# Kernel tuning notes

Hardware: AMD Instinct MI355X
Metric: run time of the kernel (lower is better)

## Reference

```python
import jax, jax.numpy as jnp
import numpy as np


def hard_sigmoid(x):
    # Keras hard_sigmoid: clip(0.2*x + 0.5, 0, 1)
    return jnp.clip(0.2 * x + 0.5, 0.0, 1.0)


def setup_inputs() -> dict:
    key = jax.random.key(0)
    k1, k2, k3 = jax.random.split(key, 3)
    B, H, W, C = 32, 64, 64, 256
    x = jax.random.normal(k1, (B, H, W, C), dtype=jnp.float32)
    # glorot_uniform over (C, W, H): fan_in = W (last-two matmul dims are W x H)
    limit = np.sqrt(6.0 / (W + H)).astype(np.float32)
    Wq = jax.random.uniform(k2, (C, W, H), minval=-limit, maxval=limit, dtype=jnp.float32)
    Wk = jax.random.uniform(k3, (C, W, H), minval=-limit, maxval=limit, dtype=jnp.float32)
    return {"x": x, "Wq": Wq, "Wk": Wk}


def reference(x, Wq, Wk):
    # x: [B, H, W, C] -> [B, C, H, W]
    xt = jnp.transpose(x, (0, 3, 1, 2))
    # projections: [B,C,H,W] @ [C,W,H] (broadcast over B) -> [B,C,H,H]
    q = hard_sigmoid(jnp.einsum('bchw,cwk->bchk', xt, Wq))
    K = jnp.tanh(jnp.einsum('bchw,cwk->bchk', xt, Wk))
    # scores: q @ K^T over last two dims -> [B,C,H,H]
    qk = hard_sigmoid(jnp.einsum('bchk,bcmk->bchm', q, K))
    qk = jax.nn.softmax(qk, axis=-1)
    # output: [B,C,H,W] @ [B,C,W(==H),H] -> [B,C,H,H]
    out = jnp.einsum('bchw,bcwm->bchm', xt, qk)
    # back to channels-last [B,H,W,C]
    return jnp.transpose(out, (0, 2, 3, 1))
```

## Files before the change

### kernel.cpp

```cpp
#include <hip/hip_runtime.h>


typedef short short8 __attribute__((ext_vector_type(8)));
typedef float floatx4 __attribute__((ext_vector_type(4)));
typedef unsigned int uint;

__device__ __forceinline__ uint cvtpk(float a, float b) {
  uint r;
  asm("v_cvt_pk_bf16_f32 %0, %1, %2" : "=v"(r) : "v"(a), "v"(b));
  return r;
}
__device__ __forceinline__ short8 u4s8(uint a, uint b, uint c, uint d) {
  union { uint u[4]; short8 s; } t;
  t.u[0] = a; t.u[1] = b; t.u[2] = c; t.u[3] = d;
  return t.s;
}
__device__ __forceinline__ float hsg(float x) {
  return fminf(fmaxf(0.2f * x + 0.5f, 0.f), 1.f);
}

__device__ __forceinline__ void pl32swap(uint A, uint C, uint& lo, uint& hi, int quad) {
#if __has_builtin(__builtin_amdgcn_permlane32_swap)
  auto r = __builtin_amdgcn_permlane32_swap(A, C, false, false);
  lo = (uint)r[0]; hi = (uint)r[1];
#else
  uint sA = __shfl_xor(A, 32), sC = __shfl_xor(C, 32);
  bool up = quad >= 2;
  lo = up ? sC : A;
  hi = up ? C : sA;
#endif
}
__device__ __forceinline__ void pl16swap(uint A, uint C, uint& lo, uint& hi, int quad) {
#if __has_builtin(__builtin_amdgcn_permlane16_swap)
  auto r = __builtin_amdgcn_permlane16_swap(A, C, false, false);
  lo = (uint)r[0]; hi = (uint)r[1];
#else
  uint sA = (uint)__builtin_amdgcn_ds_swizzle((int)A, 0x401F);
  uint sC = (uint)__builtin_amdgcn_ds_swizzle((int)C, 0x401F);
  bool odd = quad & 1;
  lo = odd ? sC : A;
  hi = odd ? C : sA;
#endif
}
__device__ __forceinline__ short8 xchg4(uint A, uint B, uint C, uint D, int quad) {
  uint Ap, Cp, Bp, Dp, t0, t1, t2, t3;
  pl32swap(A, C, Ap, Cp, quad);
  pl32swap(B, D, Bp, Dp, quad);
  pl16swap(Ap, Cp, t0, t2, quad);
  pl16swap(Bp, Dp, t1, t3, quad);
  return u4s8(t0, t1, t2, t3);
}

__global__ __launch_bounds__(256) void prep_w(const float* __restrict__ Wq,
                                              const float* __restrict__ Wk,
                                              unsigned short* __restrict__ ws) {
  __shared__ __align__(16) unsigned char sm[4 * 8704];
  const int tid = threadIdx.x, lane = tid & 63, wid = tid >> 6;
  const int task = blockIdx.x * 4 + wid;
  const int c = task & 255;
  const float* wp = ((task >> 8) ? Wk : Wq) + (size_t)c * 4096;
  unsigned char* buf = sm + wid * 8704;
  const int l15 = lane & 15, quad = lane >> 4;
#pragma unroll 4
  for (int j = 0; j < 16; ++j) {
    int f4 = j * 64 + lane;
    float4 v = *(const float4*)(wp + (size_t)f4 * 4);
    int w = f4 >> 4, k0 = (f4 & 15) << 2;
    uint2 pk; pk.x = cvtpk(v.x, v.y); pk.y = cvtpk(v.z, v.w);
    *(uint2*)(buf + w * 136 + k0 * 2) = pk;
  }
  unsigned short* dst = ws + (size_t)task * 4096;
#pragma unroll
  for (int kt = 0; kt < 4; ++kt)
#pragma unroll
    for (int ks = 0; ks < 2; ++ks) {
      const unsigned short* p = (const unsigned short*)buf + (ks * 32 + quad * 8) * 68 + (kt * 16 + l15);
      short8 af = u4s8((uint)p[0]   | ((uint)p[68]  << 16),
                       (uint)p[136] | ((uint)p[204] << 16),
                       (uint)p[272] | ((uint)p[340] << 16),
                       (uint)p[408] | ((uint)p[476] << 16));
      *(short8*)(dst + ((kt * 2 + ks) * 64 + lane) * 8) = af;
    }
}

__global__ __launch_bounds__(512, 4) void fused_attn(
    const float* __restrict__ x, const unsigned short* __restrict__ wsp,
    float* __restrict__ out) {
  __shared__ __align__(16) unsigned char smem[8 * 8192];

  const int tid  = threadIdx.x;
  const int lane = tid & 63;
  const int wid  = tid >> 6;
  const int l15  = lane & 15;
  const int quad = lane >> 4;

  const int b   = blockIdx.x & 31;
  const int cg8 = blockIdx.x >> 5;
  const int c0  = cg8 << 3;
  const int c   = c0 + wid;

  unsigned char* buf0 = smem + wid * 8192;

  const short8* wqf = (const short8*)wsp + (size_t)c * 512;
  const short8* wkf = wqf + 256 * 512;

  short8 aq[4][2];
#pragma unroll
  for (int kt = 0; kt < 4; ++kt)
#pragma unroll
    for (int ks = 0; ks < 2; ++ks) aq[kt][ks] = wqf[(kt * 2 + ks) * 64 + lane];

  {
    const int ch4 = tid & 1, grp = tid >> 1;
    const float* xb = x + (size_t)b * 4096 * 256 + c0 + ch4 * 4;
#pragma unroll
    for (int bat = 0; bat < 2; ++bat) {
      float4 va[4], vb[4];
#pragma unroll
      for (int i = 0; i < 4; ++i) {
        int pair = (bat * 4 + i) * 256 + grp;
        int h = pair >> 5, w0 = (pair & 31) << 1;
        const float* src = xb + (size_t)(h * 64 + w0) * 256;
        va[i] = *(const float4*)src;
        vb[i] = *(const float4*)(src + 256);
      }
#pragma unroll
      for (int i = 0; i < 4; ++i) {
        int pair = (bat * 4 + i) * 256 + grp;
        int h = pair >> 5, w0 = (pair & 31) << 1;
        uint off = (uint)(h * 128 + (((w0 >> 3) ^ (h & 7)) << 4) + ((w0 & 7) << 1));
        unsigned char* base = smem + (size_t)(ch4 * 4) * 8192 + off;
        *(uint*)(base + 0 * 8192) = cvtpk(va[i].x, vb[i].x);
        *(uint*)(base + 1 * 8192) = cvtpk(va[i].y, vb[i].y);
        *(uint*)(base + 2 * 8192) = cvtpk(va[i].z, vb[i].z);
        *(uint*)(base + 3 * 8192) = cvtpk(va[i].w, vb[i].w);
      }
    }
  }
  __syncthreads();

  const floatx4 zero4 = {0.f, 0.f, 0.f, 0.f};
  floatx4 acc[16];

#pragma unroll
  for (int i = 0; i < 16; ++i) acc[i] = zero4;
#pragma unroll
  for (int ht = 0; ht < 4; ++ht) {
    int r = ht * 16 + l15;
    short8 x0 = *(const short8*)(buf0 + r * 128 + (((quad) ^ (r & 7)) << 4));
    short8 x1 = *(const short8*)(buf0 + r * 128 + (((4 + quad) ^ (r & 7)) << 4));
    __builtin_amdgcn_s_setprio(1);
#pragma unroll
    for (int kt = 0; kt < 4; ++kt) {
      acc[kt * 4 + ht] = __builtin_amdgcn_mfma_f32_16x16x32_bf16(aq[kt][0], x0, acc[kt * 4 + ht], 0, 0, 0);
      acc[kt * 4 + ht] = __builtin_amdgcn_mfma_f32_16x16x32_bf16(aq[kt][1], x1, acc[kt * 4 + ht], 0, 0, 0);
    }
    __builtin_amdgcn_s_setprio(0);
  }

  short8 qf[4][2];
#pragma unroll
  for (int ht = 0; ht < 4; ++ht) {
    uint s[4][2];
#pragma unroll
    for (int kt = 0; kt < 4; ++kt) {
      floatx4 a = acc[kt * 4 + ht];
      s[kt][0] = cvtpk(hsg(a[0]), hsg(a[1]));
      s[kt][1] = cvtpk(hsg(a[2]), hsg(a[3]));
    }
#pragma unroll
    for (int ks = 0; ks < 2; ++ks)
      qf[ht][ks] = xchg4(s[2 * ks][0], s[2 * ks][1], s[2 * ks + 1][0], s[2 * ks + 1][1], quad);
  }

#pragma unroll
  for (int i = 0; i < 16; ++i) acc[i] = zero4;
#pragma unroll
  for (int kt = 0; kt < 4; ++kt) {
    short8 a0 = wkf[(kt * 2 + 0) * 64 + lane];
    short8 a1 = wkf[(kt * 2 + 1) * 64 + lane];
    __builtin_amdgcn_s_setprio(1);
#pragma unroll
    for (int ht = 0; ht < 4; ++ht) {
      int r = ht * 16 + l15;
      short8 x0 = *(const short8*)(buf0 + r * 128 + (((quad) ^ (r & 7)) << 4));
      short8 x1 = *(const short8*)(buf0 + r * 128 + (((4 + quad) ^ (r & 7)) << 4));
      acc[kt * 4 + ht] = __builtin_amdgcn_mfma_f32_16x16x32_bf16(a0, x0, acc[kt * 4 + ht], 0, 0, 0);
      acc[kt * 4 + ht] = __builtin_amdgcn_mfma_f32_16x16x32_bf16(a1, x1, acc[kt * 4 + ht], 0, 0, 0);
    }
    __builtin_amdgcn_s_setprio(0);
  }
  short8 kf[4][2];
#pragma unroll
  for (int ht = 0; ht < 4; ++ht) {
    uint t[4][2];
#pragma unroll
    for (int kt = 0; kt < 4; ++kt) {
      floatx4 a = acc[kt * 4 + ht];
      float kv[4];
#pragma unroll
      for (int i = 0; i < 4; ++i) {
        float e = __expf(2.f * a[i]);
        kv[i] = 1.f - 2.f / (e + 1.f);
      }
      t[kt][0] = cvtpk(kv[0], kv[1]);
      t[kt][1] = cvtpk(kv[2], kv[3]);
    }
#pragma unroll
    for (int ks = 0; ks < 2; ++ks)
      kf[ht][ks] = xchg4(t[2 * ks][0], t[2 * ks][1], t[2 * ks + 1][0], t[2 * ks + 1][1], quad);
  }

  short8 sf[4][2];
#pragma unroll
  for (int ks2 = 0; ks2 < 2; ++ks2) {
    floatx4 a2[8];
#pragma unroll
    for (int i = 0; i < 8; ++i) a2[i] = zero4;
    __builtin_amdgcn_s_setprio(1);
#pragma unroll
    for (int mt = 0; mt < 4; ++mt)
#pragma unroll
      for (int wtl = 0; wtl < 2; ++wtl) {
        int wt = ks2 * 2 + wtl;
        a2[wtl * 4 + mt] = __builtin_amdgcn_mfma_f32_16x16x32_bf16(qf[wt][0], kf[mt][0], a2[wtl * 4 + mt], 0, 0, 0);
        a2[wtl * 4 + mt] = __builtin_amdgcn_mfma_f32_16x16x32_bf16(qf[wt][1], kf[mt][1], a2[wtl * 4 + mt], 0, 0, 0);
      }
    __builtin_amdgcn_s_setprio(0);
#pragma unroll
    for (int i = 0; i < 8; ++i)
#pragma unroll
      for (int j = 0; j < 4; ++j) a2[i][j] = __expf(hsg(a2[i][j]));
    float inv2[2][4];
#pragma unroll
    for (int wtl = 0; wtl < 2; ++wtl)
#pragma unroll
      for (int i = 0; i < 4; ++i) {
        float pp = a2[wtl * 4 + 0][i] + a2[wtl * 4 + 1][i] + a2[wtl * 4 + 2][i] + a2[wtl * 4 + 3][i];
        pp += __shfl_xor(pp, 1, 16);
        pp += __shfl_xor(pp, 2, 16);
        pp += __shfl_xor(pp, 4, 16);
        pp += __shfl_xor(pp, 8, 16);
        inv2[wtl][i] = 1.f / pp;
      }
#pragma unroll
    for (int mt = 0; mt < 4; ++mt) {
      uint s0 = cvtpk(a2[mt][0] * inv2[0][0], a2[mt][1] * inv2[0][1]);
      uint s1 = cvtpk(a2[mt][2] * inv2[0][2], a2[mt][3] * inv2[0][3]);
      uint s2 = cvtpk(a2[4 + mt][0] * inv2[1][0], a2[4 + mt][1] * inv2[1][1]);
      uint s3 = cvtpk(a2[4 + mt][2] * inv2[1][2], a2[4 + mt][3] * inv2[1][3]);
      sf[mt][ks2] = xchg4(s0, s1, s2, s3, quad);
    }
  }

#pragma unroll
  for (int i = 0; i < 16; ++i) acc[i] = zero4;
#pragma unroll
  for (int ht = 0; ht < 4; ++ht) {
    int r = ht * 16 + l15;
    short8 x0 = *(const short8*)(buf0 + r * 128 + (((quad) ^ (r & 7)) << 4));
    short8 x1 = *(const short8*)(buf0 + r * 128 + (((4 + quad) ^ (r & 7)) << 4));
    __builtin_amdgcn_s_setprio(1);
#pragma unroll
    for (int mt = 0; mt < 4; ++mt) {
      acc[mt * 4 + ht] = __builtin_amdgcn_mfma_f32_16x16x32_bf16(sf[mt][0], x0, acc[mt * 4 + ht], 0, 0, 0);
      acc[mt * 4 + ht] = __builtin_amdgcn_mfma_f32_16x16x32_bf16(sf[mt][1], x1, acc[mt * 4 + ht], 0, 0, 0);
    }
    __builtin_amdgcn_s_setprio(0);
  }
#pragma unroll
  for (int mt = 0; mt < 4; ++mt)
#pragma unroll
    for (int ht = 0; ht < 4; ++ht) {
      floatx4 a = acc[mt * 4 + ht];
      uint2 pk; pk.x = cvtpk(a[0], a[1]); pk.y = cvtpk(a[2], a[3]);
      int h = ht * 16 + l15;
      *(uint2*)(buf0 + h * 128 + ((((mt * 2 + (quad >> 1)) ^ (h & 7))) << 4) + ((quad & 1) << 3)) = pk;
    }
  __syncthreads();

  {
    const int ch4 = tid & 1, grp = tid >> 1;
    const size_t outbase = (size_t)b * 4096 * 256 + c0 + ch4 * 4;
#pragma unroll
    for (int rep = 0; rep < 4; ++rep) {
      int qidx = rep * 256 + grp;
      int h = qidx >> 4, mq = qidx & 15;
      uint loff = (uint)(h * 128 + ((((mq >> 1) ^ (h & 7))) << 4) + ((mq & 1) << 3));
      float vals[4][4];
#pragma unroll
      for (int j = 0; j < 4; ++j) {
        uint2 d = *(const uint2*)(smem + (size_t)(ch4 * 4 + j) * 8192 + loff);
        vals[j][0] = __uint_as_float(d.x << 16);
        vals[j][1] = __uint_as_float(d.x & 0xFFFF0000u);
        vals[j][2] = __uint_as_float(d.y << 16);
        vals[j][3] = __uint_as_float(d.y & 0xFFFF0000u);
      }
      float* op = out + outbase + (size_t)(h * 64 + mq * 4) * 256;
#pragma unroll
      for (int jj = 0; jj < 4; ++jj) {
        float4 v = {vals[0][jj], vals[1][jj], vals[2][jj], vals[3][jj]};
        *(float4*)(op + (size_t)jj * 256) = v;
      }
    }
  }
}

extern "C" void kernel_launch(void* const* d_in, const int* in_sizes, int n_in,
                              void* d_out, int out_size, void* d_ws, size_t ws_size,
                              hipStream_t stream) {
  const float* x  = (const float*)d_in[0];
  const float* Wq = (const float*)d_in[1];
  const float* Wk = (const float*)d_in[2];
  unsigned short* ws = (unsigned short*)d_ws;
  prep_w<<<dim3(128), dim3(256), 0, stream>>>(Wq, Wk, ws);
  fused_attn<<<dim3(1024), dim3(512), 0, stream>>>(x, ws, (float*)d_out);
}
```

Before: 300.4 us.

## Make fused attention persistent over four batches with prefetched x staging

Each block now handles four consecutive batch items for its 8-channel group instead of one, giving 256 blocks instead of 1024. The global loads of the next batch's x slice are issued during the current batch's MFMA phases, and a separate output buffer in doubled shared memory lets staging and writeback overlap. x fragments are held in registers and reused by all three matmuls instead of being reloaded from LDS. The cost is higher register and LDS pressure (launch bounds lowered to 2 blocks per CU, 128KB LDS) and fewer blocks available to hide latency.

```diff
diff --git a/kernel.cpp b/kernel.cpp
--- a/kernel.cpp
+++ b/kernel.cpp
@@ -4,6 +4,9 @@
 typedef short short8 __attribute__((ext_vector_type(8)));
 typedef float floatx4 __attribute__((ext_vector_type(4)));
 typedef unsigned int uint;
+
+#define BAR() do { asm volatile("s_waitcnt lgkmcnt(0)" ::: "memory"); \
+    __builtin_amdgcn_s_barrier(); __builtin_amdgcn_sched_barrier(0); } while (0)
 
 __device__ __forceinline__ uint cvtpk(float a, float b) {
   uint r;
@@ -49,6 +52,41 @@
   pl16swap(Ap, Cp, t0, t2, quad);
   pl16swap(Bp, Dp, t1, t3, quad);
   return u4s8(t0, t1, t2, t3);
+}
+
+__device__ __forceinline__ void stage_issue(const float* xb, int grp, int i0,
+                                            float4* va, float4* vb) {
+#pragma unroll
+  for (int i = 0; i < 4; ++i) {
+    int pair = (i0 + i) * 256 + grp;
+    int h = pair >> 5, w0 = (pair & 31) << 1;
+    const float* src = xb + (size_t)(h * 64 + w0) * 256;
+    va[i] = *(const float4*)src;
+    vb[i] = *(const float4*)(src + 256);
+  }
+}
+__device__ __forceinline__ void stage_commit(unsigned char* base0, int grp, int i0,
+                                             const float4* va, const float4* vb) {
+#pragma unroll
+  for (int i = 0; i < 4; ++i) {
+    int pair = (i0 + i) * 256 + grp;
+    int h = pair >> 5, w0 = (pair & 31) << 1;
+    uint off = (uint)(h * 128 + (((w0 >> 3) ^ (h & 7)) << 4) + ((w0 & 7) << 1));
+    *(uint*)(base0 + 0 * 8192 + off) = cvtpk(va[i].x, vb[i].x);
+    *(uint*)(base0 + 1 * 8192 + off) = cvtpk(va[i].y, vb[i].y);
+    *(uint*)(base0 + 2 * 8192 + off) = cvtpk(va[i].z, vb[i].z);
+    *(uint*)(base0 + 3 * 8192 + off) = cvtpk(va[i].w, vb[i].w);
+  }
+}
+__device__ __forceinline__ void ld_xf(const unsigned char* buf0, int l15, int quad,
+                                      short8 xf[4][2]) {
+#pragma unroll
+  for (int rt = 0; rt < 4; ++rt) {
+    int r = rt * 16 + l15;
+#pragma unroll
+    for (int ks = 0; ks < 2; ++ks)
+      xf[rt][ks] = *(const short8*)(buf0 + r * 128 + (((ks * 4 + quad) ^ (r & 7)) << 4));
+  }
 }
 
 __global__ __launch_bounds__(256) void prep_w(const float* __restrict__ Wq,
@@ -83,23 +121,27 @@
     }
 }
 
-__global__ __launch_bounds__(512, 4) void fused_attn(
+__global__ __launch_bounds__(512, 2) void fused_attn(
     const float* __restrict__ x, const unsigned short* __restrict__ wsp,
     float* __restrict__ out) {
-  __shared__ __align__(16) unsigned char smem[8 * 8192];
+  __shared__ __align__(16) unsigned char smem[2 * 8 * 8192];
 
   const int tid  = threadIdx.x;
   const int lane = tid & 63;
   const int wid  = tid >> 6;
   const int l15  = lane & 15;
   const int quad = lane >> 4;
-
-  const int b   = blockIdx.x & 31;
-  const int cg8 = blockIdx.x >> 5;
+  const int ch4  = tid & 1;
+  const int grp  = tid >> 1;
+
+  const int cg8 = blockIdx.x & 31;
+  const int bq  = blockIdx.x >> 5;
   const int c0  = cg8 << 3;
   const int c   = c0 + wid;
 
-  unsigned char* buf0 = smem + wid * 8192;
+  unsigned char* xbuf = smem + wid * 8192;
+  unsigned char* obuf = smem + 65536 + wid * 8192;
+  unsigned char* stb  = smem + ch4 * 32768;
 
   const short8* wqf = (const short8*)wsp + (size_t)c * 512;
   const short8* wkf = wqf + 256 * 512;
@@ -111,198 +153,192 @@
     for (int ks = 0; ks < 2; ++ks) aq[kt][ks] = wqf[(kt * 2 + ks) * 64 + lane];
 
   {
-    const int ch4 = tid & 1, grp = tid >> 1;
-    const float* xb = x + (size_t)b * 4096 * 256 + c0 + ch4 * 4;
-#pragma unroll
-    for (int bat = 0; bat < 2; ++bat) {
-      float4 va[4], vb[4];
-#pragma unroll
-      for (int i = 0; i < 4; ++i) {
-        int pair = (bat * 4 + i) * 256 + grp;
-        int h = pair >> 5, w0 = (pair & 31) << 1;
-        const float* src = xb + (size_t)(h * 64 + w0) * 256;
-        va[i] = *(const float4*)src;
-        vb[i] = *(const float4*)(src + 256);
-      }
-#pragma unroll
-      for (int i = 0; i < 4; ++i) {
-        int pair = (bat * 4 + i) * 256 + grp;
-        int h = pair >> 5, w0 = (pair & 31) << 1;
-        uint off = (uint)(h * 128 + (((w0 >> 3) ^ (h & 7)) << 4) + ((w0 & 7) << 1));
-        unsigned char* base = smem + (size_t)(ch4 * 4) * 8192 + off;
-        *(uint*)(base + 0 * 8192) = cvtpk(va[i].x, vb[i].x);
-        *(uint*)(base + 1 * 8192) = cvtpk(va[i].y, vb[i].y);
-        *(uint*)(base + 2 * 8192) = cvtpk(va[i].z, vb[i].z);
-        *(uint*)(base + 3 * 8192) = cvtpk(va[i].w, vb[i].w);
-      }
-    }
-  }
-  __syncthreads();
+    const float* xb = x + (size_t)(bq * 4) * 4096 * 256 + c0 + ch4 * 4;
+    float4 va[4], vb[4];
+    stage_issue(xb, grp, 0, va, vb);
+    stage_commit(stb, grp, 0, va, vb);
+    stage_issue(xb, grp, 4, va, vb);
+    stage_commit(stb, grp, 4, va, vb);
+  }
+  BAR();
+  short8 xf[4][2];
+  ld_xf(xbuf, l15, quad, xf);
+  BAR();
 
   const floatx4 zero4 = {0.f, 0.f, 0.f, 0.f};
-  floatx4 acc[16];
-
-#pragma unroll
-  for (int i = 0; i < 16; ++i) acc[i] = zero4;
-#pragma unroll
-  for (int ht = 0; ht < 4; ++ht) {
-    int r = ht * 16 + l15;
-    short8 x0 = *(const short8*)(buf0 + r * 128 + (((quad) ^ (r & 7)) << 4));
-    short8 x1 = *(const short8*)(buf0 + r * 128 + (((4 + quad) ^ (r & 7)) << 4));
+
+  for (int it = 0; it < 4; ++it) {
+    const bool pre = (it < 3);
+    const float* xbn = x + (size_t)(bq * 4 + it + 1) * 4096 * 256 + c0 + ch4 * 4;
+    float4 va[4], vb[4];
+    if (pre) stage_issue(xbn, grp, 0, va, vb);
+
+    short8 wkr[4][2];
+#pragma unroll
+    for (int kt = 0; kt < 4; ++kt)
+#pragma unroll
+      for (int ks = 0; ks < 2; ++ks) wkr[kt][ks] = wkf[(kt * 2 + ks) * 64 + lane];
+
+    floatx4 acc[16];
+
+#pragma unroll
+    for (int i = 0; i < 16; ++i) acc[i] = zero4;
     __builtin_amdgcn_s_setprio(1);
 #pragma unroll
-    for (int kt = 0; kt < 4; ++kt) {
-      acc[kt * 4 + ht] = __builtin_amdgcn_mfma_f32_16x16x32_bf16(aq[kt][0], x0, acc[kt * 4 + ht], 0, 0, 0);
-      acc[kt * 4 + ht] = __builtin_amdgcn_mfma_f32_16x16x32_bf16(aq[kt][1], x1, acc[kt * 4 + ht], 0, 0, 0);
-    }
+    for (int kt = 0; kt < 4; ++kt)
+#pragma unroll
+      for (int ht = 0; ht < 4; ++ht) {
+        acc[kt * 4 + ht] = __builtin_amdgcn_mfma_f32_16x16x32_bf16(aq[kt][0], xf[ht][0], acc[kt * 4 + ht], 0, 0, 0);
+        acc[kt * 4 + ht] = __builtin_amdgcn_mfma_f32_16x16x32_bf16(aq[kt][1], xf[ht][1], acc[kt * 4 + ht], 0, 0, 0);
+      }
     __builtin_amdgcn_s_setprio(0);
-  }
-
-  short8 qf[4][2];
-#pragma unroll
-  for (int ht = 0; ht < 4; ++ht) {
-    uint s[4][2];
-#pragma unroll
-    for (int kt = 0; kt < 4; ++kt) {
-      floatx4 a = acc[kt * 4 + ht];
-      s[kt][0] = cvtpk(hsg(a[0]), hsg(a[1]));
-      s[kt][1] = cvtpk(hsg(a[2]), hsg(a[3]));
-    }
-#pragma unroll
-    for (int ks = 0; ks < 2; ++ks)
-      qf[ht][ks] = xchg4(s[2 * ks][0], s[2 * ks][1], s[2 * ks + 1][0], s[2 * ks + 1][1], quad);
-  }
-
-#pragma unroll
-  for (int i = 0; i < 16; ++i) acc[i] = zero4;
-#pragma unroll
-  for (int kt = 0; kt < 4; ++kt) {
-    short8 a0 = wkf[(kt * 2 + 0) * 64 + lane];
-    short8 a1 = wkf[(kt * 2 + 1) * 64 + lane];
+
+    short8 qf[4][2];
+#pragma unroll
+    for (int ht = 0; ht < 4; ++ht) {
+      uint s[4][2];
+#pragma unroll
+      for (int kt = 0; kt < 4; ++kt) {
+        floatx4 a = acc[kt * 4 + ht];
+        s[kt][0] = cvtpk(hsg(a[0]), hsg(a[1]));
+        s[kt][1] = cvtpk(hsg(a[2]), hsg(a[3]));
+      }
+#pragma unroll
+      for (int ks = 0; ks < 2; ++ks)
+        qf[ht][ks] = xchg4(s[2 * ks][0], s[2 * ks][1], s[2 * ks + 1][0], s[2 * ks + 1][1], quad);
+    }
+
+    if (pre) {
+      stage_commit(stb, grp, 0, va, vb);
+      stage_issue(xbn, grp, 4, va, vb);
+    }
+
+#pragma unroll
+    for (int i = 0; i < 16; ++i) acc[i] = zero4;
     __builtin_amdgcn_s_setprio(1);
 #pragma unroll
+    for (int kt = 0; kt < 4; ++kt)
+#pragma unroll
+      for (int ht = 0; ht < 4; ++ht) {
+        acc[kt * 4 + ht] = __builtin_amdgcn_mfma_f32_16x16x32_bf16(wkr[kt][0], xf[ht][0], acc[kt * 4 + ht], 0, 0, 0);
+        acc[kt * 4 + ht] = __builtin_amdgcn_mfma_f32_16x16x32_bf16(wkr[kt][1], xf[ht][1], acc[kt * 4 + ht], 0, 0, 0);
+      }
+    __builtin_amdgcn_s_setprio(0);
+
+    short8 kf[4][2];
+#pragma unroll
     for (int ht = 0; ht < 4; ++ht) {
-      int r = ht * 16 + l15;
-      short8 x0 = *(const short8*)(buf0 + r * 128 + (((quad) ^ (r & 7)) << 4));
-      short8 x1 = *(const short8*)(buf0 + r * 128 + (((4 + quad) ^ (r & 7)) << 4));
-      acc[kt * 4 + ht] = __builtin_amdgcn_mfma_f32_16x16x32_bf16(a0, x0, acc[kt * 4 + ht], 0, 0, 0);
-      acc[kt * 4 + ht] = __builtin_amdgcn_mfma_f32_16x16x32_bf16(a1, x1, acc[kt * 4 + ht], 0, 0, 0);
-    }
+      uint t[4][2];
+#pragma unroll
+      for (int kt = 0; kt < 4; ++kt) {
+        floatx4 a = acc[kt * 4 + ht];
+        float kv[4];
+#pragma unroll
+        for (int i = 0; i < 4; ++i) {
+          float e = __expf(2.f * a[i]);
+          kv[i] = 1.f - 2.f / (e + 1.f);
+        }
+        t[kt][0] = cvtpk(kv[0], kv[1]);
+        t[kt][1] = cvtpk(kv[2], kv[3]);
+      }
+#pragma unroll
+      for (int ks = 0; ks < 2; ++ks)
+        kf[ht][ks] = xchg4(t[2 * ks][0], t[2 * ks][1], t[2 * ks + 1][0], t[2 * ks + 1][1], quad);
+    }
+
+    if (pre) stage_commit(stb, grp, 4, va, vb);
+
+    short8 sf[4][2];
+#pragma unroll
+    for (int ks2 = 0; ks2 < 2; ++ks2) {
+      floatx4 a2[8];
+#pragma unroll
+      for (int i = 0; i < 8; ++i) a2[i] = zero4;
+      __builtin_amdgcn_s_setprio(1);
+#pragma unroll
+      for (int mt = 0; mt < 4; ++mt)
+#pragma unroll
+        for (int wtl = 0; wtl < 2; ++wtl) {
+          int wt = ks2 * 2 + wtl;
+          a2[wtl * 4 + mt] = __builtin_amdgcn_mfma_f32_16x16x32_bf16(qf[wt][0], kf[mt][0], a2[wtl * 4 + mt], 0, 0, 0);
+          a2[wtl * 4 + mt] = __builtin_amdgcn_mfma_f32_16x16x32_bf16(qf[wt][1], kf[mt][1], a2[wtl * 4 + mt], 0, 0, 0);
+        }
+      __builtin_amdgcn_s_setprio(0);
+#pragma unroll
+      for (int i = 0; i < 8; ++i)
+#pragma unroll
+        for (int j = 0; j < 4; ++j) a2[i][j] = __expf(hsg(a2[i][j]));
+      float inv2[2][4];
+#pragma unroll
+      for (int wtl = 0; wtl < 2; ++wtl)
+#pragma unroll
+        for (int i = 0; i < 4; ++i) {
+          float pp = a2[wtl * 4 + 0][i] + a2[wtl * 4 + 1][i] + a2[wtl * 4 + 2][i] + a2[wtl * 4 + 3][i];
+          pp += __shfl_xor(pp, 1, 16);
+          pp += __shfl_xor(pp, 2, 16);
+          pp += __shfl_xor(pp, 4, 16);
+          pp += __shfl_xor(pp, 8, 16);
+          inv2[wtl][i] = 1.f / pp;
+        }
+#pragma unroll
+      for (int mt = 0; mt < 4; ++mt) {
+        uint s0 = cvtpk(a2[mt][0] * inv2[0][0], a2[mt][1] * inv2[0][1]);
+        uint s1 = cvtpk(a2[mt][2] * inv2[0][2], a2[mt][3] * inv2[0][3]);
+        uint s2 = cvtpk(a2[4 + mt][0] * inv2[1][0], a2[4 + mt][1] * inv2[1][1]);
+        uint s3 = cvtpk(a2[4 + mt][2] * inv2[1][2], a2[4 + mt][3] * inv2[1][3]);
+        sf[mt][ks2] = xchg4(s0, s1, s2, s3, quad);
+      }
+    }
+
+#pragma unroll
+    for (int i = 0; i < 16; ++i) acc[i] = zero4;
+    __builtin_amdgcn_s_setprio(1);
+#pragma unroll
+    for (int mt = 0; mt < 4; ++mt)
+#pragma unroll
+      for (int ht = 0; ht < 4; ++ht) {
+        acc[mt * 4 + ht] = __builtin_amdgcn_mfma_f32_16x16x32_bf16(sf[mt][0], xf[ht][0], acc[mt * 4 + ht], 0, 0, 0);
+        acc[mt * 4 + ht] = __builtin_amdgcn_mfma_f32_16x16x32_bf16(sf[mt][1], xf[ht][1], acc[mt * 4 + ht], 0, 0, 0);
+      }
     __builtin_amdgcn_s_setprio(0);
-  }
-  short8 kf[4][2];
-#pragma unroll
-  for (int ht = 0; ht < 4; ++ht) {
-    uint t[4][2];
-#pragma unroll
-    for (int kt = 0; kt < 4; ++kt) {
-      floatx4 a = acc[kt * 4 + ht];
-      float kv[4];
-#pragma unroll
-      for (int i = 0; i < 4; ++i) {
-        float e = __expf(2.f * a[i]);
-        kv[i] = 1.f - 2.f / (e + 1.f);
-      }
-      t[kt][0] = cvtpk(kv[0], kv[1]);
-      t[kt][1] = cvtpk(kv[2], kv[3]);
-    }
-#pragma unroll
-    for (int ks = 0; ks < 2; ++ks)
-      kf[ht][ks] = xchg4(t[2 * ks][0], t[2 * ks][1], t[2 * ks + 1][0], t[2 * ks + 1][1], quad);
-  }
-
-  short8 sf[4][2];
-#pragma unroll
-  for (int ks2 = 0; ks2 < 2; ++ks2) {
-    floatx4 a2[8];
-#pragma unroll
-    for (int i = 0; i < 8; ++i) a2[i] = zero4;
-    __builtin_amdgcn_s_setprio(1);
 #pragma unroll
     for (int mt = 0; mt < 4; ++mt)
 #pragma unroll
-      for (int wtl = 0; wtl < 2; ++wtl) {
-        int wt = ks2 * 2 + wtl;
-        a2[wtl * 4 + mt] = __builtin_amdgcn_mfma_f32_16x16x32_bf16(qf[wt][0], kf[mt][0], a2[wtl * 4 + mt], 0, 0, 0);
-        a2[wtl * 4 + mt] = __builtin_amdgcn_mfma_f32_16x16x32_bf16(qf[wt][1], kf[mt][1], a2[wtl * 4 + mt], 0, 0, 0);
-      }
-    __builtin_amdgcn_s_setprio(0);
-#pragma unroll
-    for (int i = 0; i < 8; ++i)
-#pragma unroll
-      for (int j = 0; j < 4; ++j) a2[i][j] = __expf(hsg(a2[i][j]));
-    float inv2[2][4];
-#pragma unroll
-    for (int wtl = 0; wtl < 2; ++wtl)
-#pragma unroll
-      for (int i = 0; i < 4; ++i) {
-        float pp = a2[wtl * 4 + 0][i] + a2[wtl * 4 + 1][i] + a2[wtl * 4 + 2][i] + a2[wtl * 4 + 3][i];
-        pp += __shfl_xor(pp, 1, 16);
-        pp += __shfl_xor(pp, 2, 16);
-        pp += __shfl_xor(pp, 4, 16);
-        pp += __shfl_xor(pp, 8, 16);
-        inv2[wtl][i] = 1.f / pp;
-      }
-#pragma unroll
-    for (int mt = 0; mt < 4; ++mt) {
-      uint s0 = cvtpk(a2[mt][0] * inv2[0][0], a2[mt][1] * inv2[0][1]);
-      uint s1 = cvtpk(a2[mt][2] * inv2[0][2], a2[mt][3] * inv2[0][3]);
-      uint s2 = cvtpk(a2[4 + mt][0] * inv2[1][0], a2[4 + mt][1] * inv2[1][1]);
-      uint s3 = cvtpk(a2[4 + mt][2] * inv2[1][2], a2[4 + mt][3] * inv2[1][3]);
-      sf[mt][ks2] = xchg4(s0, s1, s2, s3, quad);
-    }
-  }
-
-#pragma unroll
-  for (int i = 0; i < 16; ++i) acc[i] = zero4;
-#pragma unroll
-  for (int ht = 0; ht < 4; ++ht) {
-    int r = ht * 16 + l15;
-    short8 x0 = *(const short8*)(buf0 + r * 128 + (((quad) ^ (r & 7)) << 4));
-    short8 x1 = *(const short8*)(buf0 + r * 128 + (((4 + quad) ^ (r & 7)) << 4));
-    __builtin_amdgcn_s_setprio(1);
-#pragma unroll
-    for (int mt = 0; mt < 4; ++mt) {
-      acc[mt * 4 + ht] = __builtin_amdgcn_mfma_f32_16x16x32_bf16(sf[mt][0], x0, acc[mt * 4 + ht], 0, 0, 0);
-      acc[mt * 4 + ht] = __builtin_amdgcn_mfma_f32_16x16x32_bf16(sf[mt][1], x1, acc[mt * 4 + ht], 0, 0, 0);
-    }
-    __builtin_amdgcn_s_setprio(0);
-  }
-#pragma unroll
-  for (int mt = 0; mt < 4; ++mt)
-#pragma unroll
-    for (int ht = 0; ht < 4; ++ht) {
-      floatx4 a = acc[mt * 4 + ht];
-      uint2 pk; pk.x = cvtpk(a[0], a[1]); pk.y = cvtpk(a[2], a[3]);
-      int h = ht * 16 + l15;
-      *(uint2*)(buf0 + h * 128 + ((((mt * 2 + (quad >> 1)) ^ (h & 7))) << 4) + ((quad & 1) << 3)) = pk;
-    }
-  __syncthreads();
-
-  {
-    const int ch4 = tid & 1, grp = tid >> 1;
-    const size_t outbase = (size_t)b * 4096 * 256 + c0 + ch4 * 4;
-#pragma unroll
-    for (int rep = 0; rep < 4; ++rep) {
-      int qidx = rep * 256 + grp;
-      int h = qidx >> 4, mq = qidx & 15;
-      uint loff = (uint)(h * 128 + ((((mq >> 1) ^ (h & 7))) << 4) + ((mq & 1) << 3));
-      float vals[4][4];
-#pragma unroll
-      for (int j = 0; j < 4; ++j) {
-        uint2 d = *(const uint2*)(smem + (size_t)(ch4 * 4 + j) * 8192 + loff);
-        vals[j][0] = __uint_as_float(d.x << 16);
-        vals[j][1] = __uint_as_float(d.x & 0xFFFF0000u);
-        vals[j][2] = __uint_as_float(d.y << 16);
-        vals[j][3] = __uint_as_float(d.y & 0xFFFF0000u);
-      }
-      float* op = out + outbase + (size_t)(h * 64 + mq * 4) * 256;
-#pragma unroll
-      for (int jj = 0; jj < 4; ++jj) {
-        float4 v = {vals[0][jj], vals[1][jj], vals[2][jj], vals[3][jj]};
-        *(float4*)(op + (size_t)jj * 256) = v;
-      }
-    }
+      for (int ht = 0; ht < 4; ++ht) {
+        floatx4 a = acc[mt * 4 + ht];
+        uint2 pk; pk.x = cvtpk(a[0], a[1]); pk.y = cvtpk(a[2], a[3]);
+        int h = ht * 16 + l15;
+        *(uint2*)(obuf + h * 128 + ((((mt * 2 + (quad >> 1)) ^ (h & 7))) << 4) + ((quad & 1) << 3)) = pk;
+      }
+    BAR();
+
+    if (pre) ld_xf(xbuf, l15, quad, xf);
+
+    {
+      const size_t outbase = (size_t)(bq * 4 + it) * 4096 * 256 + c0 + ch4 * 4;
+#pragma unroll
+      for (int rep = 0; rep < 4; ++rep) {
+        int qidx = rep * 256 + grp;
+        int h = qidx >> 4, mq = qidx & 15;
+        uint loff = (uint)(h * 128 + ((((mq >> 1) ^ (h & 7))) << 4) + ((mq & 1) << 3));
+        float vals[4][4];
+#pragma unroll
+        for (int j = 0; j < 4; ++j) {
+          uint2 d = *(const uint2*)(smem + 65536 + (size_t)(ch4 * 4 + j) * 8192 + loff);
+          vals[j][0] = __uint_as_float(d.x << 16);
+          vals[j][1] = __uint_as_float(d.x & 0xFFFF0000u);
+          vals[j][2] = __uint_as_float(d.y << 16);
+          vals[j][3] = __uint_as_float(d.y & 0xFFFF0000u);
+        }
+        float* op = out + outbase + (size_t)(h * 64 + mq * 4) * 256;
+#pragma unroll
+        for (int jj = 0; jj < 4; ++jj) {
+          float4 v = {vals[0][jj], vals[1][jj], vals[2][jj], vals[3][jj]};
+          *(float4*)(op + (size_t)jj * 256) = v;
+        }
+      }
+    }
+    BAR();
   }
 }
 
@@ -314,5 +350,5 @@
   const float* Wk = (const float*)d_in[2];
   unsigned short* ws = (unsigned short*)d_ws;
   prep_w<<<dim3(128), dim3(256), 0, stream>>>(Wq, Wk, ws);
-  fused_attn<<<dim3(1024), dim3(512), 0, stream>>>(x, ws, (float*)d_out);
-}
+  fused_attn<<<dim3(256), dim3(512), 0, stream>>>(x, ws, (float*)d_out);
+}
```

Result: slower. 362.9 us (+20.8%).
